# Kernel optimization log

Hardware: AMD Instinct MI355X
Metric: run time of the kernel (lower is better)

The kernel has to match this reference:

```python
import jax, jax.numpy as jnp
import numpy as np
import math

V, BLOCK, D, L, H, B, T = 32000, 1024, 1024, 6, 16, 4, 1024
HD = D // H
FF = 4 * D


def setup_inputs() -> dict:
    key = jax.random.key(0)
    ks = jax.random.split(key, 16)
    s = 0.02
    inp = {
        "idx": jax.random.randint(ks[0], (B, T), 0, V),
        "tok_emb": s * jax.random.normal(ks[1], (V, D), jnp.float32),
        "pos_emb": jnp.zeros((1, BLOCK, D), jnp.float32) + s * jax.random.normal(ks[2], (1, BLOCK, D), jnp.float32),
        "ln1_g": jnp.ones((L, D), jnp.float32),
        "ln1_b": jnp.zeros((L, D), jnp.float32),
        "qkv_w": s * jax.random.normal(ks[3], (L, 3 * D, D), jnp.float32),
        "proj_w": s * jax.random.normal(ks[4], (L, D, D), jnp.float32),
        "ln2_g": jnp.ones((L, D), jnp.float32),
        "ln2_b": jnp.zeros((L, D), jnp.float32),
        "mlp_w1": s * jax.random.normal(ks[5], (L, FF, D), jnp.float32),
        "mlp_b1": jnp.zeros((L, FF), jnp.float32),
        "mlp_w2": s * jax.random.normal(ks[6], (L, D, FF), jnp.float32),
        "mlp_b2": jnp.zeros((L, D), jnp.float32),
        "lnf_g": jnp.ones((D,), jnp.float32),
        "lnf_b": jnp.zeros((D,), jnp.float32),
        "head_w": s * jax.random.normal(ks[7], (V, D), jnp.float32),
    }
    return inp


def _layernorm(x, g, b, eps=1e-5):
    mu = jnp.mean(x, axis=-1, keepdims=True)
    var = jnp.mean(jnp.square(x - mu), axis=-1, keepdims=True)
    return (x - mu) * jax.lax.rsqrt(var + eps) * g + b


def _attn(x, qkv_w, proj_w):
    b, t, c = x.shape
    qkv = jnp.einsum('btc,fc->btf', x, qkv_w)  # [B,T,3D]
    q, k, v = jnp.split(qkv, 3, axis=-1)
    q = q.reshape(b, t, H, HD)
    k = k.reshape(b, t, H, HD)
    v = v.reshape(b, t, H, HD)
    att = jnp.einsum('bqhd,bkhd->bhqk', q, k) / math.sqrt(HD)
    causal = jnp.tril(jnp.ones((t, t), bool))
    att = jnp.where(causal[None, None], att, -jnp.inf)
    att = jax.nn.softmax(att, axis=-1)
    y = jnp.einsum('bhqk,bkhd->bqhd', att, v).reshape(b, t, c)
    return jnp.einsum('btc,fc->btf', y, proj_w)


def reference(idx, tok_emb, pos_emb, ln1_g, ln1_b, qkv_w, proj_w,
              ln2_g, ln2_b, mlp_w1, mlp_b1, mlp_w2, mlp_b2,
              lnf_g, lnf_b, head_w):
    t = idx.shape[1]
    x = tok_emb[idx] + pos_emb[:, :t, :]
    for i in range(L):
        h = _layernorm(x, ln1_g[i], ln1_b[i])
        x = x + _attn(h, qkv_w[i], proj_w[i])
        h = _layernorm(x, ln2_g[i], ln2_b[i])
        h = jax.nn.gelu(jnp.einsum('btc,fc->btf', h, mlp_w1[i]) + mlp_b1[i], approximate=False)
        x = x + jnp.einsum('btf,cf->btc', h, mlp_w2[i]) + mlp_b2[i]
    x = _layernorm(x, lnf_g, lnf_b)
    logits = jnp.einsum('btc,vc->btv', x, head_w)
    return logits
```

## Files before the change

### kernel.cpp

```cpp
#include <hip/hip_runtime.h>
#include <hip/hip_bf16.h>
#include <math.h>

#define BB 4
#define TT 1024
#define DD 1024
#define HH 16
#define HDIM 64
#define FFD 4096
#define VV 32000
#define LL 6
#define BT (BB * TT)

typedef __bf16 bf16;
typedef bf16 bf16x8 __attribute__((ext_vector_type(8)));
typedef bf16 bf16x4 __attribute__((ext_vector_type(4)));
typedef float f32x4 __attribute__((ext_vector_type(4)));

__device__ __forceinline__ void gload16(const void* g, void* l) {
    __builtin_amdgcn_global_load_lds((__attribute__((address_space(1))) unsigned int*)(g),
                                     (__attribute__((address_space(3))) unsigned int*)(l),
                                     16, 0, 0);
}

__global__ __launch_bounds__(256) void embed_k(const int* __restrict__ idx,
                                               const float* __restrict__ tok,
                                               const float* __restrict__ pos,
                                               float* __restrict__ x) {
    int row = blockIdx.x;
    int tid = threadIdx.x;
    int t = row & (TT - 1);
    int token = idx[row];
    float4 a = *(const float4*)(tok + (size_t)token * DD + tid * 4);
    float4 p = *(const float4*)(pos + (size_t)t * DD + tid * 4);
    *(float4*)(x + (size_t)row * DD + tid * 4) =
        make_float4(a.x + p.x, a.y + p.y, a.z + p.z, a.w + p.w);
}

__global__ __launch_bounds__(256) void cvt_bf16_k(const float* __restrict__ in,
                                                  bf16* __restrict__ out, long n) {
    long i0 = ((long)blockIdx.x * 256 + threadIdx.x) * 8;
    long stride = (long)gridDim.x * 256 * 8;
    for (long i = i0; i < n; i += stride) {
        float4 v0 = *(const float4*)(in + i);
        float4 v1 = *(const float4*)(in + i + 4);
        bf16x8 o;
        o[0] = (bf16)v0.x; o[1] = (bf16)v0.y; o[2] = (bf16)v0.z; o[3] = (bf16)v0.w;
        o[4] = (bf16)v1.x; o[5] = (bf16)v1.y; o[6] = (bf16)v1.z; o[7] = (bf16)v1.w;
        *(bf16x8*)(out + i) = o;
    }
}

__global__ __launch_bounds__(256) void layernorm_k(const float* __restrict__ in,
                                                   bf16* __restrict__ out,
                                                   const float* __restrict__ g,
                                                   const float* __restrict__ b) {
    __shared__ float red[256];
    int row = blockIdx.x;
    int tid = threadIdx.x;
    const float* ip = in + (size_t)row * DD;
    float4 v = *(const float4*)(ip + tid * 4);

    float s = v.x + v.y + v.z + v.w;
    red[tid] = s; __syncthreads();
    for (int st = 128; st > 0; st >>= 1) { if (tid < st) red[tid] += red[tid + st]; __syncthreads(); }
    float mu = red[0] * (1.0f / DD);
    __syncthreads();

    float d0 = v.x - mu, d1 = v.y - mu, d2 = v.z - mu, d3 = v.w - mu;
    red[tid] = d0 * d0 + d1 * d1 + d2 * d2 + d3 * d3; __syncthreads();
    for (int st = 128; st > 0; st >>= 1) { if (tid < st) red[tid] += red[tid + st]; __syncthreads(); }
    float var = red[0] * (1.0f / DD);
    float rs = rsqrtf(var + 1e-5f);

    float4 gv = *(const float4*)(g + tid * 4);
    float4 bv = *(const float4*)(b + tid * 4);
    bf16x4 o;
    o[0] = (bf16)(d0 * rs * gv.x + bv.x);
    o[1] = (bf16)(d1 * rs * gv.y + bv.y);
    o[2] = (bf16)(d2 * rs * gv.z + bv.z);
    o[3] = (bf16)(d3 * rs * gv.w + bv.w);
    *(bf16x4*)(out + (size_t)row * DD + tid * 4) = o;
}

template <bool BIAS, bool GELU, bool OBF>
__global__ __launch_bounds__(512, 2) void gemm_256(const bf16* __restrict__ A,
                                                   const bf16* __restrict__ W,
                                                   const float* __restrict__ bias,
                                                   void* __restrict__ Cv,
                                                   int M, int N, int K) {
    __shared__ char lds[2 * 65536];
    const int tid = threadIdx.x;
    const int lane = tid & 63, wave = tid >> 6;
    const int c = lane & 15, g = lane >> 4;

    const int nm = M >> 8;
    const int nwg = gridDim.x;
    const int wgid = (blockIdx.x & 7) * (nwg >> 3) + (blockIdx.x >> 3);
    const int m0 = (wgid % nm) * 256, n0 = (wgid / nm) * 256;
    const int wm = wave >> 2, wn = wave & 3;

    const int srow = tid >> 2;
    const int lq = (tid & 3) ^ ((tid >> 3) & 3);
    const bf16* Asrc = A + (size_t)(m0 + srow) * K + lq * 8;
    const bf16* Bsrc = W + (size_t)(n0 + srow) * K + lq * 8;
    const size_t K128 = (size_t)128 * K;

    const int key = (c >> 1) & 3;
    const int rdA = (wm * 128 + c) * 64 + ((g ^ key) * 16);
    const int rdB = 32768 + (wn * 64 + c) * 64 + ((g ^ key) * 16);

    f32x4 acc[8][4] = {};
    const int NT = K >> 6;
    const int NH = 4 * NT;

#define STAGEH(H)                                                             \
    if ((H) < NH) {                                                           \
        const int t2_ = (H) >> 2, h_ = (H) & 3;                               \
        const bf16* s_ = ((h_ & 1) ? Bsrc : Asrc) + (size_t)t2_ * 64 + (h_ >> 1) * 32; \
        char* d_ = lds + (t2_ & 1) * 65536 + (h_ & 1) * 32768 + (h_ >> 1) * 16384 + tid * 16; \
        gload16(s_, d_);                                                      \
        gload16(s_ + K128, d_ + 8192);                                        \
    }

#define MFMA16(base)                                                          \
    __builtin_amdgcn_s_setprio(1);                                            \
    _Pragma("unroll")                                                         \
    for (int fi = 0; fi < 4; ++fi) {                                          \
        _Pragma("unroll")                                                     \
        for (int fj = 0; fj < 4; ++fj)                                        \
            acc[(base) + fi][fj] = __builtin_amdgcn_mfma_f32_16x16x32_bf16(   \
                bA[fi], bB[fj], acc[(base) + fi][fj], 0, 0, 0);               \
    }                                                                         \
    __builtin_amdgcn_s_setprio(0);

    STAGEH(0); STAGEH(1); STAGEH(2); STAGEH(3); STAGEH(4);
    asm volatile("s_waitcnt vmcnt(6)" ::: "memory");
    __builtin_amdgcn_sched_barrier(0);
    __builtin_amdgcn_s_barrier();
    __builtin_amdgcn_sched_barrier(0);

    for (int kt = 0; kt < NT; ++kt) {
        const char* bp = lds + (kt & 1) * 65536;
        bf16x8 bA[4], bB[4];
#pragma unroll
        for (int fj = 0; fj < 4; ++fj) bB[fj] = *(const bf16x8*)(bp + rdB + fj * 1024);
#pragma unroll
        for (int fi = 0; fi < 4; ++fi) bA[fi] = *(const bf16x8*)(bp + rdA + fi * 1024);
        STAGEH(4 * kt + 5);
        __builtin_amdgcn_s_barrier();
        asm volatile("s_waitcnt lgkmcnt(0)" ::: "memory");
        __builtin_amdgcn_sched_barrier(0);
        MFMA16(0)
        __builtin_amdgcn_s_barrier();
        __builtin_amdgcn_sched_barrier(0);
#pragma unroll
        for (int fi = 0; fi < 4; ++fi) bA[fi] = *(const bf16x8*)(bp + rdA + (4 + fi) * 1024);
        STAGEH(4 * kt + 6);
        __builtin_amdgcn_s_barrier();
        asm volatile("s_waitcnt lgkmcnt(0)" ::: "memory");
        __builtin_amdgcn_sched_barrier(0);
        MFMA16(4)
        if (kt + 1 < NT) { asm volatile("s_waitcnt vmcnt(6)" ::: "memory"); }
        else             { asm volatile("s_waitcnt vmcnt(0)" ::: "memory"); }
        __builtin_amdgcn_sched_barrier(0);
        __builtin_amdgcn_s_barrier();
        __builtin_amdgcn_sched_barrier(0);
#pragma unroll
        for (int fj = 0; fj < 4; ++fj) bB[fj] = *(const bf16x8*)(bp + rdB + 16384 + fj * 1024);
#pragma unroll
        for (int fi = 0; fi < 4; ++fi) bA[fi] = *(const bf16x8*)(bp + rdA + 16384 + fi * 1024);
        STAGEH(4 * kt + 7);
        __builtin_amdgcn_s_barrier();
        asm volatile("s_waitcnt lgkmcnt(0)" ::: "memory");
        __builtin_amdgcn_sched_barrier(0);
        MFMA16(0)
        __builtin_amdgcn_s_barrier();
        __builtin_amdgcn_sched_barrier(0);
#pragma unroll
        for (int fi = 0; fi < 4; ++fi) bA[fi] = *(const bf16x8*)(bp + rdA + 16384 + (4 + fi) * 1024);
        STAGEH(4 * kt + 8);
        __builtin_amdgcn_s_barrier();
        asm volatile("s_waitcnt lgkmcnt(0)" ::: "memory");
        __builtin_amdgcn_sched_barrier(0);
        MFMA16(4)
        if (kt + 2 < NT)      { asm volatile("s_waitcnt vmcnt(6)" ::: "memory"); }
        else if (kt + 2 == NT){ asm volatile("s_waitcnt vmcnt(4)" ::: "memory"); }
        __builtin_amdgcn_sched_barrier(0);
        __builtin_amdgcn_s_barrier();
        __builtin_amdgcn_sched_barrier(0);
    }
#undef STAGEH
#undef MFMA16

    const int orow  = m0 + wm * 128 + g * 4;
    const int ocol0 = n0 + wn * 64 + c;
#pragma unroll
    for (int fj = 0; fj < 4; ++fj) {
        const int col = ocol0 + fj * 16;
        float bs = 0.f;
        if (BIAS) bs = bias[col];
#pragma unroll
        for (int fi = 0; fi < 8; ++fi) {
#pragma unroll
            for (int r = 0; r < 4; ++r) {
                int row = orow + fi * 16 + r;
                float v = acc[fi][fj][r] + bs;
                if (GELU) v = 0.5f * v * (1.0f + erff(v * 0.70710678118654752f));
                if (OBF) ((bf16*)Cv)[(size_t)row * N + col] = (bf16)v;
                else     ((float*)Cv)[(size_t)row * N + col] = v;
            }
        }
    }
}

template <bool ADD, bool BIAS, bool GELU, bool OBF>
__global__ __launch_bounds__(256) void gemm_mfma(const bf16* __restrict__ A,
                                                 const bf16* __restrict__ W,
                                                 const float* __restrict__ bias,
                                                 void* __restrict__ Cv,
                                                 int M, int N, int K) {
    __shared__ bf16 As[128 * 32];
    __shared__ bf16 Ws[128 * 32];
    const int tid  = threadIdx.x;
    const int wave = tid >> 6, lane = tid & 63;

    const int nm = M >> 7;
    const int nwg = gridDim.x;
    const int wgid = (blockIdx.x & 7) * (nwg >> 3) + (blockIdx.x >> 3);
    const int m0 = (wgid % nm) * 128, n0 = (wgid / nm) * 128;

    const int wm = (wave >> 1) * 64, wn = (wave & 1) * 64;

    const int srow = wave * 16 + (lane >> 2);
    const int sk   = (lane & 3) * 8;
    const bf16* Ag = A + (size_t)(m0 + srow) * K + sk;
    const bf16* Wg = W + (size_t)(n0 + srow) * K + sk;
    char* lA = (char*)As + wave * 1024;
    char* lW = (char*)Ws + wave * 1024;

    const int rl = lane & 15, kg = lane >> 4;
    const bf16* Ard = As + (size_t)(wm + rl) * 32 + kg * 8;
    const bf16* Wrd = Ws + (size_t)(wn + rl) * 32 + kg * 8;

    f32x4 acc[4][4] = {};

    for (int k0 = 0; k0 < K; k0 += 32) {
        gload16(Ag + k0,                   lA);
        gload16(Ag + k0 + (size_t)64 * K,  lA + 4096);
        gload16(Wg + k0,                   lW);
        gload16(Wg + k0 + (size_t)64 * K,  lW + 4096);
        __syncthreads();
        bf16x8 a[4], b[4];
#pragma unroll
        for (int i = 0; i < 4; ++i) a[i] = *(const bf16x8*)(Ard + i * 16 * 32);
#pragma unroll
        for (int j = 0; j < 4; ++j) b[j] = *(const bf16x8*)(Wrd + j * 16 * 32);
#pragma unroll
        for (int i = 0; i < 4; ++i)
#pragma unroll
            for (int j = 0; j < 4; ++j)
                acc[i][j] = __builtin_amdgcn_mfma_f32_16x16x32_bf16(a[i], b[j], acc[i][j], 0, 0, 0);
        __syncthreads();
    }

    const int orow  = m0 + wm + (lane >> 4) * 4;
    const int ocol0 = n0 + wn + (lane & 15);
#pragma unroll
    for (int j = 0; j < 4; ++j) {
        const int col = ocol0 + j * 16;
        float bs = 0.f;
        if (BIAS) bs = bias[col];
#pragma unroll
        for (int i = 0; i < 4; ++i) {
#pragma unroll
            for (int r = 0; r < 4; ++r) {
                int row = orow + i * 16 + r;
                float v = acc[i][j][r] + bs;
                if (GELU) v = 0.5f * v * (1.0f + erff(v * 0.70710678118654752f));
                if (OBF) {
                    ((bf16*)Cv)[(size_t)row * N + col] = (bf16)v;
                } else {
                    float* p = (float*)Cv + (size_t)row * N + col;
                    if (ADD) *p += v; else *p = v;
                }
            }
        }
    }
}

__global__ __launch_bounds__(256) void vprep_k(const bf16* __restrict__ qkv,
                                               bf16* __restrict__ Vt) {
    __shared__ bf16 Vls[64 * 72];
    const int tid = threadIdx.x;
    const int t0 = blockIdx.x * 64;
    const int h = blockIdx.y, b = blockIdx.z;
    const int row = tid >> 3, ch = tid & 7;

    const bf16* src = qkv + ((size_t)(b * TT + t0 + row)) * 3072 + 2048 + h * 64 + ch * 8;
    bf16x8 v0 = *(const bf16x8*)(src);
    bf16x8 v1 = *(const bf16x8*)(src + (size_t)32 * 3072);
#pragma unroll
    for (int j = 0; j < 8; ++j) {
        Vls[(ch * 8 + j) * 72 + row]      = v0[j];
        Vls[(ch * 8 + j) * 72 + row + 32] = v1[j];
    }
    __syncthreads();

    const int dr = tid >> 3;
    bf16* dst = Vt + ((size_t)((b * HH + h) * 64 + dr)) * 1024 + t0 + ch * 8;
    bf16x8 o0 = *(const bf16x8*)(Vls + dr * 72 + ch * 8);
    bf16x8 o1 = *(const bf16x8*)(Vls + (dr + 32) * 72 + ch * 8);
    *(bf16x8*)(dst) = o0;
    *(bf16x8*)(dst + (size_t)32 * 1024) = o1;
}

__global__ __launch_bounds__(256) void fattn_k(const bf16* __restrict__ qkv,
                                               const bf16* __restrict__ Vt,
                                               bf16* __restrict__ y) {
    __shared__ bf16 Ks[2][64 * 64];
    __shared__ bf16 Vs[2][64 * 64];
    __shared__ bf16 Ps[4][16 * 72];
    const int tid = threadIdx.x, lane = tid & 63, wave = tid >> 6;
    const int g = lane >> 4, c = lane & 15;
    const int q0 = blockIdx.x * 64;
    const int h = blockIdx.y, b = blockIdx.z;
    const size_t qbase = (size_t)b * TT * 3072;

    const int qrow = q0 + wave * 16 + c;
    const bf16* qp = qkv + qbase + (size_t)qrow * 3072 + h * 64;
    bf16x8 qf0 = *(const bf16x8*)(qp + g * 8);
    bf16x8 qf1 = *(const bf16x8*)(qp + 32 + g * 8);

    const int srow = tid >> 3;
    const int lq = (tid & 7) ^ (srow & 7);
    const bf16* Ksrc = qkv + qbase + 1024 + h * 64 + (size_t)srow * 3072 + lq * 8;
    const bf16* Vsrc = Vt + ((size_t)(b * HH + h) * 64 + srow) * 1024 + lq * 8;

    float mO[4] = {-1e30f, -1e30f, -1e30f, -1e30f};
    float lO[4] = {0.f, 0.f, 0.f, 0.f};
    f32x4 acc[4] = {};

    bf16* pw = Ps[wave];
    const int ntiles = blockIdx.x + 1;
    const int qg0 = q0 + wave * 16 + 4 * g;
    const int cs = c & 7;

#define STAGE_KV(t_, buf_)                                                        \
    {                                                                             \
        const int kk_ = (t_) * 64;                                                \
        gload16(Ksrc + (size_t)kk_ * 3072,        (char*)Ks[buf_] + tid * 16);    \
        gload16(Ksrc + (size_t)(kk_ + 32) * 3072, (char*)Ks[buf_] + tid * 16 + 4096); \
        gload16(Vsrc + kk_,                       (char*)Vs[buf_] + tid * 16);    \
        gload16(Vsrc + 32 * 1024 + kk_,           (char*)Vs[buf_] + tid * 16 + 4096); \
    }

    STAGE_KV(0, 0)

    for (int t = 0; t < ntiles; ++t) {
        const int k0 = t * 64;
        if (t + 1 < ntiles) {
            STAGE_KV(t + 1, (t + 1) & 1)
            asm volatile("s_waitcnt vmcnt(4)" ::: "memory");
        } else {
            asm volatile("s_waitcnt vmcnt(0)" ::: "memory");
        }
        __builtin_amdgcn_sched_barrier(0);
        __builtin_amdgcn_s_barrier();
        __builtin_amdgcn_sched_barrier(0);

        const bf16* kb = Ks[t & 1];
        const bf16* vb = Vs[t & 1];

        f32x4 s[4] = {};
#pragma unroll
        for (int j = 0; j < 4; ++j) {
            const bf16* kr = kb + (16 * j + c) * 64;
            bf16x8 kf0 = *(const bf16x8*)(kr + ((g ^ cs) * 8));
            bf16x8 kf1 = *(const bf16x8*)(kr + (((4 + g) ^ cs) * 8));
            s[j] = __builtin_amdgcn_mfma_f32_16x16x32_bf16(qf0, kf0, s[j], 0, 0, 0);
            s[j] = __builtin_amdgcn_mfma_f32_16x16x32_bf16(qf1, kf1, s[j], 0, 0, 0);
        }

        float mt_[4];
        bool need = false;
#pragma unroll
        for (int r = 0; r < 4; ++r) {
            const int qg = qg0 + r;
            float a0 = s[0][r] * 0.125f, a1 = s[1][r] * 0.125f;
            float a2 = s[2][r] * 0.125f, a3 = s[3][r] * 0.125f;
            if (k0 + c > qg)      a0 = -1e30f;
            if (k0 + 16 + c > qg) a1 = -1e30f;
            if (k0 + 32 + c > qg) a2 = -1e30f;
            if (k0 + 48 + c > qg) a3 = -1e30f;
            s[0][r] = a0; s[1][r] = a1; s[2][r] = a2; s[3][r] = a3;
            float mt = fmaxf(fmaxf(a0, a1), fmaxf(a2, a3));
            mt = fmaxf(mt, __shfl_xor(mt, 1));
            mt = fmaxf(mt, __shfl_xor(mt, 2));
            mt = fmaxf(mt, __shfl_xor(mt, 4));
            mt = fmaxf(mt, __shfl_xor(mt, 8));
            mt_[r] = mt;
            need |= (mt > mO[r]);
        }
        if (__any(need)) {
#pragma unroll
            for (int r = 0; r < 4; ++r) {
                float mn = fmaxf(mO[r], mt_[r]);
                float sc = __expf(mO[r] - mn);
                mO[r] = mn;
                lO[r] *= sc;
                acc[0][r] *= sc; acc[1][r] *= sc; acc[2][r] *= sc; acc[3][r] *= sc;
            }
        }
#pragma unroll
        for (int r = 0; r < 4; ++r) {
            float e0 = __expf(s[0][r] - mO[r]);
            float e1 = __expf(s[1][r] - mO[r]);
            float e2 = __expf(s[2][r] - mO[r]);
            float e3 = __expf(s[3][r] - mO[r]);
            lO[r] += (e0 + e1) + (e2 + e3);
            bf16* pr = pw + (4 * g + r) * 72;
            pr[c] = (bf16)e0; pr[16 + c] = (bf16)e1;
            pr[32 + c] = (bf16)e2; pr[48 + c] = (bf16)e3;
        }

#pragma unroll
        for (int ks = 0; ks < 2; ++ks) {
            bf16x8 pf = *(const bf16x8*)(pw + c * 72 + ks * 32 + g * 8);
#pragma unroll
            for (int jb = 0; jb < 4; ++jb) {
                const int d = 16 * jb + c;
                bf16x8 vf = *(const bf16x8*)(vb + d * 64 + (((ks * 4 + g) ^ cs) * 8));
                acc[jb] = __builtin_amdgcn_mfma_f32_16x16x32_bf16(pf, vf, acc[jb], 0, 0, 0);
            }
        }
        __builtin_amdgcn_s_barrier();
        __builtin_amdgcn_sched_barrier(0);
    }
#undef STAGE_KV

#pragma unroll
    for (int r = 0; r < 4; ++r) {
        float l = lO[r];
        l += __shfl_xor(l, 1);
        l += __shfl_xor(l, 2);
        l += __shfl_xor(l, 4);
        l += __shfl_xor(l, 8);
        float invl = 1.0f / l;
        size_t orow = (size_t)(b * TT + qg0 + r) * DD + h * 64;
#pragma unroll
        for (int jb = 0; jb < 4; ++jb)
            y[orow + jb * 16 + c] = (bf16)(acc[jb][r] * invl);
    }
}

extern "C" void kernel_launch(void* const* d_in, const int* in_sizes, int n_in,
                              void* d_out, int out_size, void* d_ws, size_t ws_size,
                              hipStream_t stream) {
    const int*   idx     = (const int*)d_in[0];
    const float* tok_emb = (const float*)d_in[1];
    const float* pos_emb = (const float*)d_in[2];
    const float* ln1_g   = (const float*)d_in[3];
    const float* ln1_b   = (const float*)d_in[4];
    const float* qkv_w   = (const float*)d_in[5];
    const float* proj_w  = (const float*)d_in[6];
    const float* ln2_g   = (const float*)d_in[7];
    const float* ln2_b   = (const float*)d_in[8];
    const float* mlp_w1  = (const float*)d_in[9];
    const float* mlp_b1  = (const float*)d_in[10];
    const float* mlp_w2  = (const float*)d_in[11];
    const float* mlp_b2  = (const float*)d_in[12];
    const float* lnf_g   = (const float*)d_in[13];
    const float* lnf_b   = (const float*)d_in[14];
    const float* head_w  = (const float*)d_in[15];
    float* out = (float*)d_out;

    char* ws = (char*)d_ws;
    float* x      = (float*)ws;
    bf16*  qkv_bf = (bf16*)(ws + (16ull << 20));
    bf16*  Vt     = (bf16*)(ws + (40ull << 20));
    bf16*  h_bf   = (bf16*)(ws + (48ull << 20));
    bf16*  y_bf   = (bf16*)(ws + (56ull << 20));
    bf16*  ff_bf  = (bf16*)(ws + (64ull << 20));
    bf16*  wbuf   = (bf16*)(ws + (96ull << 20));
    bf16*  hw_bf  = (bf16*)(ws + (56ull << 20));

    embed_k<<<BT, 256, 0, stream>>>(idx, tok_emb, pos_emb, x);

    for (int l = 0; l < LL; ++l) {
        layernorm_k<<<BT, 256, 0, stream>>>(x, h_bf, ln1_g + (size_t)l * DD, ln1_b + (size_t)l * DD);
        cvt_bf16_k<<<2048, 256, 0, stream>>>(qkv_w + (size_t)l * 3 * DD * DD, wbuf, (long)3 * DD * DD);
        gemm_256<false, false, true><<<(BT / 256) * (3 * DD / 256), 512, 0, stream>>>(
            h_bf, wbuf, nullptr, qkv_bf, BT, 3 * DD, DD);
        vprep_k<<<dim3(TT / 64, HH, BB), 256, 0, stream>>>(qkv_bf, Vt);
        fattn_k<<<dim3(TT / 64, HH, BB), 256, 0, stream>>>(qkv_bf, Vt, y_bf);
        cvt_bf16_k<<<2048, 256, 0, stream>>>(proj_w + (size_t)l * DD * DD, wbuf, (long)DD * DD);
        gemm_mfma<true, false, false, false><<<(BT / 128) * (DD / 128), 256, 0, stream>>>(
            y_bf, wbuf, nullptr, x, BT, DD, DD);
        layernorm_k<<<BT, 256, 0, stream>>>(x, h_bf, ln2_g + (size_t)l * DD, ln2_b + (size_t)l * DD);
        cvt_bf16_k<<<2048, 256, 0, stream>>>(mlp_w1 + (size_t)l * FFD * DD, wbuf, (long)FFD * DD);
        gemm_256<true, true, true><<<(BT / 256) * (FFD / 256), 512, 0, stream>>>(
            h_bf, wbuf, mlp_b1 + (size_t)l * FFD, ff_bf, BT, FFD, DD);
        cvt_bf16_k<<<2048, 256, 0, stream>>>(mlp_w2 + (size_t)l * DD * FFD, wbuf, (long)DD * FFD);
        gemm_mfma<true, true, false, false><<<(BT / 128) * (DD / 128), 256, 0, stream>>>(
            ff_bf, wbuf, mlp_b2 + (size_t)l * DD, x, BT, DD, FFD);
    }

    layernorm_k<<<BT, 256, 0, stream>>>(x, h_bf, lnf_g, lnf_b);
    cvt_bf16_k<<<4096, 256, 0, stream>>>(head_w, hw_bf, (long)VV * DD);
    gemm_256<false, false, false><<<(BT / 256) * (VV / 256), 512, 0, stream>>>(
        h_bf, hw_bf, nullptr, out, BT, VV, DD);
}
```

Before: 2.367 ms.

## Pipeline 128x128 GEMM with double-buffered LDS and reverse attention block order

Replaces the simple 128x128 MFMA GEMM used for the projection and MLP-down layers with a double-buffered version. It stages K in 64-wide tiles, prefetches ahead with async global-to-LDS loads, uses an XOR-swizzled LDS layout, raises MFMA priority and adds occupancy hints. This is meant to hide global load latency behind MFMA work instead of syncing on every K step. Separately, flash attention now launches the query blocks with the most key tiles first, so the causal workload is better balanced across the GPU. The hand-placed waitcnt and barrier sequence is fragile and relies on exact counts of outstanding loads.

New measurement: 2.067 ms. -12.6%, faster.

```diff
diff --git a/kernel.cpp b/kernel.cpp
--- a/kernel.cpp
+++ b/kernel.cpp
@@ -214,76 +214,113 @@
     }
 }
 
-template <bool ADD, bool BIAS, bool GELU, bool OBF>
-__global__ __launch_bounds__(256) void gemm_mfma(const bf16* __restrict__ A,
-                                                 const bf16* __restrict__ W,
-                                                 const float* __restrict__ bias,
-                                                 void* __restrict__ Cv,
-                                                 int M, int N, int K) {
-    __shared__ bf16 As[128 * 32];
-    __shared__ bf16 Ws[128 * 32];
-    const int tid  = threadIdx.x;
-    const int wave = tid >> 6, lane = tid & 63;
+template <bool ADD, bool BIAS>
+__global__ __launch_bounds__(256, 2) void gemm_128p(const bf16* __restrict__ A,
+                                                    const bf16* __restrict__ W,
+                                                    const float* __restrict__ bias,
+                                                    float* __restrict__ C,
+                                                    int M, int N, int K) {
+    __shared__ char lds[2 * 32768];
+    const int tid = threadIdx.x;
+    const int lane = tid & 63, wave = tid >> 6;
+    const int c = lane & 15, g = lane >> 4;
 
     const int nm = M >> 7;
     const int nwg = gridDim.x;
     const int wgid = (blockIdx.x & 7) * (nwg >> 3) + (blockIdx.x >> 3);
     const int m0 = (wgid % nm) * 128, n0 = (wgid / nm) * 128;
-
-    const int wm = (wave >> 1) * 64, wn = (wave & 1) * 64;
-
-    const int srow = wave * 16 + (lane >> 2);
-    const int sk   = (lane & 3) * 8;
-    const bf16* Ag = A + (size_t)(m0 + srow) * K + sk;
-    const bf16* Wg = W + (size_t)(n0 + srow) * K + sk;
-    char* lA = (char*)As + wave * 1024;
-    char* lW = (char*)Ws + wave * 1024;
-
-    const int rl = lane & 15, kg = lane >> 4;
-    const bf16* Ard = As + (size_t)(wm + rl) * 32 + kg * 8;
-    const bf16* Wrd = Ws + (size_t)(wn + rl) * 32 + kg * 8;
+    const int wm = wave >> 1, wn = wave & 1;
+
+    const int srow = tid >> 2;
+    const int lq = (tid & 3) ^ ((tid >> 3) & 3);
+    const bf16* Asrc = A + (size_t)(m0 + srow) * K + lq * 8;
+    const bf16* Bsrc = W + (size_t)(n0 + srow) * K + lq * 8;
+    const size_t K64 = (size_t)64 * K;
+
+    const int key = (c >> 1) & 3;
+    const int rdA = (wm * 64 + c) * 64 + ((g ^ key) * 16);
+    const int rdB = 16384 + (wn * 64 + c) * 64 + ((g ^ key) * 16);
 
     f32x4 acc[4][4] = {};
-
-    for (int k0 = 0; k0 < K; k0 += 32) {
-        gload16(Ag + k0,                   lA);
-        gload16(Ag + k0 + (size_t)64 * K,  lA + 4096);
-        gload16(Wg + k0,                   lW);
-        gload16(Wg + k0 + (size_t)64 * K,  lW + 4096);
-        __syncthreads();
-        bf16x8 a[4], b[4];
-#pragma unroll
-        for (int i = 0; i < 4; ++i) a[i] = *(const bf16x8*)(Ard + i * 16 * 32);
-#pragma unroll
-        for (int j = 0; j < 4; ++j) b[j] = *(const bf16x8*)(Wrd + j * 16 * 32);
-#pragma unroll
-        for (int i = 0; i < 4; ++i)
-#pragma unroll
-            for (int j = 0; j < 4; ++j)
-                acc[i][j] = __builtin_amdgcn_mfma_f32_16x16x32_bf16(a[i], b[j], acc[i][j], 0, 0, 0);
-        __syncthreads();
-    }
-
-    const int orow  = m0 + wm + (lane >> 4) * 4;
-    const int ocol0 = n0 + wn + (lane & 15);
-#pragma unroll
-    for (int j = 0; j < 4; ++j) {
-        const int col = ocol0 + j * 16;
+    const int NT = K >> 6;
+    const int NH = 4 * NT;
+
+#define STAGEH(H)                                                             \
+    if ((H) < NH) {                                                           \
+        const int t2_ = (H) >> 2, h_ = (H) & 3;                               \
+        const bf16* s_ = ((h_ & 1) ? Bsrc : Asrc) + (size_t)t2_ * 64 + (h_ >> 1) * 32; \
+        char* d_ = lds + (t2_ & 1) * 32768 + (h_ & 1) * 16384 + (h_ >> 1) * 8192 + tid * 16; \
+        gload16(s_, d_);                                                      \
+        gload16(s_ + K64, d_ + 4096);                                         \
+    }
+
+#define MFMA16()                                                              \
+    __builtin_amdgcn_s_setprio(1);                                            \
+    _Pragma("unroll")                                                         \
+    for (int fi = 0; fi < 4; ++fi) {                                          \
+        _Pragma("unroll")                                                     \
+        for (int fj = 0; fj < 4; ++fj)                                        \
+            acc[fi][fj] = __builtin_amdgcn_mfma_f32_16x16x32_bf16(            \
+                bA[fi], bB[fj], acc[fi][fj], 0, 0, 0);                        \
+    }                                                                         \
+    __builtin_amdgcn_s_setprio(0);
+
+    STAGEH(0); STAGEH(1); STAGEH(2); STAGEH(3); STAGEH(4); STAGEH(5);
+    asm volatile("s_waitcnt vmcnt(8)" ::: "memory");
+    __builtin_amdgcn_sched_barrier(0);
+    __builtin_amdgcn_s_barrier();
+    __builtin_amdgcn_sched_barrier(0);
+
+    for (int kt = 0; kt < NT; ++kt) {
+        const char* bp = lds + (kt & 1) * 32768;
+        bf16x8 bA[4], bB[4];
+#pragma unroll
+        for (int fj = 0; fj < 4; ++fj) bB[fj] = *(const bf16x8*)(bp + rdB + fj * 1024);
+#pragma unroll
+        for (int fi = 0; fi < 4; ++fi) bA[fi] = *(const bf16x8*)(bp + rdA + fi * 1024);
+        STAGEH(4 * kt + 6); STAGEH(4 * kt + 7);
+        __builtin_amdgcn_s_barrier();
+        asm volatile("s_waitcnt lgkmcnt(0)" ::: "memory");
+        __builtin_amdgcn_sched_barrier(0);
+        MFMA16()
+        if (kt + 1 < NT) { asm volatile("s_waitcnt vmcnt(8)" ::: "memory"); }
+        else             { asm volatile("s_waitcnt vmcnt(0)" ::: "memory"); }
+        __builtin_amdgcn_sched_barrier(0);
+        __builtin_amdgcn_s_barrier();
+        __builtin_amdgcn_sched_barrier(0);
+#pragma unroll
+        for (int fj = 0; fj < 4; ++fj) bB[fj] = *(const bf16x8*)(bp + rdB + 8192 + fj * 1024);
+#pragma unroll
+        for (int fi = 0; fi < 4; ++fi) bA[fi] = *(const bf16x8*)(bp + rdA + 8192 + fi * 1024);
+        STAGEH(4 * kt + 8); STAGEH(4 * kt + 9);
+        __builtin_amdgcn_s_barrier();
+        asm volatile("s_waitcnt lgkmcnt(0)" ::: "memory");
+        __builtin_amdgcn_sched_barrier(0);
+        MFMA16()
+        if (kt + 2 < NT)       { asm volatile("s_waitcnt vmcnt(8)" ::: "memory"); }
+        else if (kt + 2 == NT) { asm volatile("s_waitcnt vmcnt(4)" ::: "memory"); }
+        __builtin_amdgcn_sched_barrier(0);
+        __builtin_amdgcn_s_barrier();
+        __builtin_amdgcn_sched_barrier(0);
+    }
+#undef STAGEH
+#undef MFMA16
+
+    const int orow  = m0 + wm * 64 + g * 4;
+    const int ocol0 = n0 + wn * 64 + c;
+#pragma unroll
+    for (int fj = 0; fj < 4; ++fj) {
+        const int col = ocol0 + fj * 16;
         float bs = 0.f;
         if (BIAS) bs = bias[col];
 #pragma unroll
-        for (int i = 0; i < 4; ++i) {
+        for (int fi = 0; fi < 4; ++fi) {
 #pragma unroll
             for (int r = 0; r < 4; ++r) {
-                int row = orow + i * 16 + r;
-                float v = acc[i][j][r] + bs;
-                if (GELU) v = 0.5f * v * (1.0f + erff(v * 0.70710678118654752f));
-                if (OBF) {
-                    ((bf16*)Cv)[(size_t)row * N + col] = (bf16)v;
-                } else {
-                    float* p = (float*)Cv + (size_t)row * N + col;
-                    if (ADD) *p += v; else *p = v;
-                }
+                int row = orow + fi * 16 + r;
+                float v = acc[fi][fj][r] + bs;
+                float* p = C + (size_t)row * N + col;
+                if (ADD) *p += v; else *p = v;
             }
         }
     }
@@ -323,7 +360,7 @@
     __shared__ bf16 Ps[4][16 * 72];
     const int tid = threadIdx.x, lane = tid & 63, wave = tid >> 6;
     const int g = lane >> 4, c = lane & 15;
-    const int q0 = blockIdx.x * 64;
+    const int q0 = (gridDim.x - 1 - blockIdx.x) * 64;
     const int h = blockIdx.y, b = blockIdx.z;
     const size_t qbase = (size_t)b * TT * 3072;
 
@@ -342,7 +379,7 @@
     f32x4 acc[4] = {};
 
     bf16* pw = Ps[wave];
-    const int ntiles = blockIdx.x + 1;
+    const int ntiles = (q0 >> 6) + 1;
     const int qg0 = q0 + wave * 16 + 4 * g;
     const int cs = c & 7;
 
@@ -495,14 +532,14 @@
         vprep_k<<<dim3(TT / 64, HH, BB), 256, 0, stream>>>(qkv_bf, Vt);
         fattn_k<<<dim3(TT / 64, HH, BB), 256, 0, stream>>>(qkv_bf, Vt, y_bf);
         cvt_bf16_k<<<2048, 256, 0, stream>>>(proj_w + (size_t)l * DD * DD, wbuf, (long)DD * DD);
-        gemm_mfma<true, false, false, false><<<(BT / 128) * (DD / 128), 256, 0, stream>>>(
+        gemm_128p<true, false><<<(BT / 128) * (DD / 128), 256, 0, stream>>>(
             y_bf, wbuf, nullptr, x, BT, DD, DD);
         layernorm_k<<<BT, 256, 0, stream>>>(x, h_bf, ln2_g + (size_t)l * DD, ln2_b + (size_t)l * DD);
         cvt_bf16_k<<<2048, 256, 0, stream>>>(mlp_w1 + (size_t)l * FFD * DD, wbuf, (long)FFD * DD);
         gemm_256<true, true, true><<<(BT / 256) * (FFD / 256), 512, 0, stream>>>(
             h_bf, wbuf, mlp_b1 + (size_t)l * FFD, ff_bf, BT, FFD, DD);
         cvt_bf16_k<<<2048, 256, 0, stream>>>(mlp_w2 + (size_t)l * DD * FFD, wbuf, (long)DD * FFD);
-        gemm_mfma<true, true, false, false><<<(BT / 128) * (DD / 128), 256, 0, stream>>>(
+        gemm_128p<true, true><<<(BT / 128) * (DD / 128), 256, 0, stream>>>(
             ff_bf, wbuf, mlp_b2 + (size_t)l * DD, x, BT, DD, FFD);
     }
 
```
